# Kernel optimization log

Hardware: AMD Instinct MI355X
Metric: run time of the kernel (lower is better)

## Reference

```python
import jax, jax.numpy as jnp
import numpy as np

KH, KW = 2, 2          # kernel_size
STH, STW = 2, 2        # stride
NW = KH * KW           # num wires (qubits) per patch
DIM = 2 ** NW          # Hilbert-space dim = 16


def setup_inputs() -> dict:
    key = jax.random.key(0)
    k1, k2 = jax.random.split(key)
    x = jax.random.normal(k1, (32, 4, 64, 64), dtype=jnp.float32)
    # learned parameter: [in_channels, out_channels//numwires, 2^NW, 2^NW]
    params = jax.random.normal(k2, (4, 8, DIM, DIM), dtype=jnp.float32)
    return {"x": x, "params": params}


def _extract_patches(x):
    # x: [B, C, H, W] -> [B, C, px, py, KH*KW] (row-major kh,kw ordering,
    # matching patches.permute(0,1,4,5,2,3).flatten(4) in the original)
    B, C, H, W = x.shape
    px = (H - KH) // STH + 1
    py = (W - KW) // STW + 1
    rows = (jnp.arange(px) * STH)[:, None] + jnp.arange(KH)  # [px, KH]
    cols = (jnp.arange(py) * STW)[:, None] + jnp.arange(KW)  # [py, KW]
    p = x[:, :, rows][:, :, :, :, cols]        # [B, C, px, KH, py, KW]
    p = p.transpose(0, 1, 2, 4, 3, 5)          # [B, C, px, py, KH, KW]
    return p.reshape(B, C, px, py, NW), px, py


def _forward(x, params):
    B, C, H, W = x.shape
    p, px, py = _extract_patches(x)
    M = B * px * py
    theta = p.transpose(1, 0, 2, 3, 4).reshape(C, M, NW)  # 'b c px py i -> c (b px py) i'

    # Encode: the original builds the full tensor-product of per-wire RX
    # matrices and contracts with |0...0>, which selects row 0 of the Kronecker
    # product. Row 0 of RX(theta) is [cos(t/2), -i sin(t/2)], so the encoded
    # state is the Kronecker product of the per-wire row-0 vectors (same math,
    # without materializing the [C,M,16,16] unitary).
    half = theta * 0.5
    v = (jnp.cos(half).astype(jnp.complex64)[..., None] * jnp.array([1.0, 0.0], jnp.complex64)
         + jnp.sin(half).astype(jnp.complex64)[..., None] * jnp.array([0.0, -1.0j], jnp.complex64))  # [C,M,NW,2]
    state = v[:, :, 0]                                     # [C, M, 2]
    for w in range(1, NW):
        state = (state[..., :, None] * v[:, :, w][..., None, :]).reshape(C, M, -1)
    # state: [C, M, DIM]

    # Skew-Hermitian generator: real part antisymmetric, imag part symmetric.
    sym = params + params.swapaxes(-1, -2)
    asym = params - params.swapaxes(-1, -2)
    SH = asym.astype(jnp.complex64) + 1j * sym.astype(jnp.complex64)  # [C, D, DIM, DIM]
    U = jax.vmap(jax.vmap(jax.scipy.linalg.expm))(SH)                 # [C, D, DIM, DIM]

    y = jnp.einsum('cdij,cmi->cdmj', U, state)  # [C, D, M, DIM]

    # Decode: per-wire marginal probabilities -> <sigma_z>-style expectation -> acos
    probs = (y * jnp.conj(y)).real              # [C, D, M, DIM]
    D = probs.shape[1]
    outs = []
    for j in range(NW):
        marg = probs.reshape(C, D, M, 2 ** j, 2, 2 ** (NW - j - 1)).sum(axis=(3, 5))  # [C,D,M,2]
        outs.append(jnp.arccos(marg[..., 0] - marg[..., 1]))
    out = jnp.stack(outs, -1)                   # [C, D, M, NW]
    out = out.sum(0)                            # [D, M, NW]  (sum over in_channels)

    # 'c (b px py) (x y) -> b (c x y) px py' with c=D, x=KH, y=KW
    out = out.reshape(D, B, px, py, KH, KW).transpose(1, 0, 4, 5, 2, 3)
    return out.reshape(B, D * KH * KW, px, py)  # [B, out_channels, px, py]


def reference(x, params):
    return _forward(x, params)
```

## Files before the change

kernel.cpp:

```cpp
#include <hip/hip_runtime.h>
#include <math.h>


typedef __attribute__((ext_vector_type(8)))  short bf16x8;
typedef __attribute__((ext_vector_type(16))) float f32x16;

__device__ __forceinline__ unsigned bfr(float x) {
    unsigned u = __float_as_uint(x);
    return (u + 0x7FFFu + ((u >> 16) & 1u)) >> 16;
}

__device__ __forceinline__ void mm16(float2* D, const float2* A, const float2* B,
                                     int i, int j, int tid) {
    float accr = 0.f, acci = 0.f;
    #pragma unroll
    for (int t = 0; t < 16; ++t) {
        float2 a = A[i * 16 + t], b = B[t * 16 + j];
        accr += a.x * b.x - a.y * b.y;
        acci += a.x * b.y + a.y * b.x;
    }
    D[tid] = make_float2(accr, acci);
    __syncthreads();
}

__device__ __forceinline__ void mm16_addb(float2* D, const float2* A, const float2* B,
                                          const float2* X1, const float2* X2c,
                                          const float2* X3c,
                                          float b0, float b1, float b2, float b3,
                                          int i, int j, int tid) {
    float accr = 0.f, acci = 0.f;
    #pragma unroll
    for (int t = 0; t < 16; ++t) {
        float2 a = A[i * 16 + t], b = B[t * 16 + j];
        accr += a.x * b.x - a.y * b.y;
        acci += a.x * b.y + a.y * b.x;
    }
    float2 v1 = X1[tid], v2 = X2c[tid], v3 = X3c[tid];
    float idd = (i == j) ? 1.f : 0.f;
    accr += b0 * idd + b1 * v1.x + b2 * v2.x + b3 * v3.x;
    acci +=            b1 * v1.y + b2 * v2.y + b3 * v3.y;
    D[tid] = make_float2(accr, acci);
    __syncthreads();
}

__global__ __launch_bounds__(256) void prep_kernel(const float* __restrict__ params,
                                                   unsigned* __restrict__ wfrag) {
    __shared__ float2 Xs[256], X2[256], X3[256], X4[256], PA[256], PB[256];
    __shared__ float red[256];
    __shared__ float srow[16];
    __shared__ int ssexp;

    const int bid = blockIdx.x;
    const int tid = threadIdx.x;
    const int i = tid >> 4, j = tid & 15;

    const float* pm = params + bid * 256;
    float pij = pm[i * 16 + j];
    float pji = pm[j * 16 + i];
    float ar = pij - pji;
    float ai = pij + pji;
    red[tid] = fabsf(ar) + fabsf(ai);
    __syncthreads();
    if (j == 0) {
        float s = 0.f;
        for (int t = 0; t < 16; ++t) s += red[i * 16 + t];
        srow[i] = s;
    }
    __syncthreads();
    if (tid == 0) {
        float mx = 0.f;
        for (int t = 0; t < 16; ++t) mx = fmaxf(mx, srow[t]);
        int se = 0;
        while (mx > 1.0f && se < 40) { mx *= 0.5f; se++; }
        ssexp = se;
    }
    __syncthreads();
    const int sexp = ssexp;
    const float scale = exp2f((float)(-sexp));
    Xs[tid] = make_float2(ar * scale, ai * scale);
    __syncthreads();

    mm16(X2, Xs, Xs, i, j, tid);
    mm16(X3, X2, Xs, i, j, tid);
    mm16(X4, X2, X2, i, j, tid);

    {
        const float c8 = 2.4801587e-5f, c9 = 2.7557319e-6f, c10 = 2.7557319e-7f,
                    c11 = 2.5052108e-8f, c12 = 2.0876757e-9f;
        float2 v1 = Xs[tid], v2 = X2[tid], v3 = X3[tid], v4 = X4[tid];
        float idd = (i == j) ? 1.f : 0.f;
        PA[tid] = make_float2(c8 * idd + c9 * v1.x + c10 * v2.x + c11 * v3.x + c12 * v4.x,
                              c9 * v1.y + c10 * v2.y + c11 * v3.y + c12 * v4.y);
        __syncthreads();
    }
    mm16_addb(PB, X4, PA, Xs, X2, X3,
              4.1666667e-2f, 8.3333333e-3f, 1.3888889e-3f, 1.9841270e-4f, i, j, tid);
    mm16_addb(PA, X4, PB, Xs, X2, X3,
              1.f, 1.f, 0.5f, 1.6666667e-1f, i, j, tid);

    float2* cur = PA;
    float2* nxt = PB;
    for (int sq = 0; sq < sexp; ++sq) {
        float accr = 0.f, acci = 0.f;
        #pragma unroll
        for (int t = 0; t < 16; ++t) {
            float2 a = cur[i * 16 + t], b = cur[t * 16 + j];
            accr += a.x * b.x - a.y * b.y;
            acci += a.x * b.y + a.y * b.x;
        }
        nxt[tid] = make_float2(accr, acci);
        __syncthreads();
        float2* tmp = cur; cur = nxt; nxt = tmp;
    }

    float2 e = cur[tid];
    int pc = __popc(i) & 3;
    float2 o;
    if (pc == 0)      o = make_float2( e.x,  e.y);
    else if (pc == 1) o = make_float2( e.y, -e.x);
    else if (pc == 2) o = make_float2(-e.x, -e.y);
    else              o = make_float2(-e.y,  e.x);
    Xs[(tid & 15) * 16 + (tid >> 4)] = o;
    __syncthreads();

    {
        const int lane = tid & 63;
        const int pr = tid >> 6;
        const int row = lane & 31;
        const int kh = lane >> 5;
        const int k0 = kh * 8 + pr * 2;
        float v0, v1;
        if (row < 16) { v0 = Xs[row * 16 + k0].x; v1 = Xs[row * 16 + k0 + 1].x; }
        else          { v0 = Xs[(row - 16) * 16 + k0].y; v1 = Xs[(row - 16) * 16 + k0 + 1].y; }
        unsigned base = (unsigned)(bid * 64 + lane) * 4u;
        wfrag[base + pr] = bfr(v0) | (bfr(v1) << 16);
    }
}

__device__ __forceinline__ float acos_fast(float t) {
    float ax = fabsf(t);
    float p = fmaf(ax, -0.0187293f, 0.0742610f);
    p = fmaf(ax, p, -0.2121144f);
    p = fmaf(ax, p, 1.5707288f);
    float f = sqrtf(1.0f - ax) * p;
    return (t >= 0.f) ? f : (3.14159265358979f - f);
}

__global__ __launch_bounds__(256)
__attribute__((amdgpu_waves_per_eu(2, 4)))
void qconv_kernel(const float* __restrict__ x,
                  const unsigned* __restrict__ wfrag,
                  float* __restrict__ out) {
    const int tid = threadIdx.x;
    const int lane = tid & 63;
    const int s = lane & 31;
    const int hi = lane >> 5;
    const int wave = blockIdx.x * 4 + (tid >> 6);
    const int msite = wave >> 1;
    const int dh = wave & 1;
    const int m = msite * 32 + s;
    const int b = m >> 10, ix = (m >> 5) & 31, iy = m & 31;

    const bf16x8* wf = (const bf16x8*)wfrag;

    float2 xa[4], xb[4];
    #pragma unroll
    for (int c = 0; c < 4; ++c) {
        const float* xc = x + (((b * 4 + c) * 64 + 2 * ix) * 64 + 2 * iy);
        xa[c] = *(const float2*)xc;
        xb[c] = *(const float2*)(xc + 64);
    }
    bf16x8 wfr[16];
    #pragma unroll
    for (int dd = 0; dd < 4; ++dd)
        #pragma unroll
        for (int c = 0; c < 4; ++c)
            wfr[dd * 4 + c] = wf[(c * 8 + dh * 4 + dd) * 64 + lane];

    bf16x8 bhi[4], blo[4];
    #pragma unroll
    for (int c = 0; c < 4; ++c) {
        float sn0, cs0, sn1, cs1, sn2, cs2, sn3, cs3;
        __sincosf(xa[c].x * 0.5f, &sn0, &cs0);
        __sincosf(xa[c].y * 0.5f, &sn1, &cs1);
        __sincosf(xb[c].x * 0.5f, &sn2, &cs2);
        __sincosf(xb[c].y * 0.5f, &sn3, &cs3);
        float f0 = hi ? sn0 : cs0;
        float g0 = f0 * cs1, g1 = f0 * sn1;
        float h0 = g0 * cs2, h1 = g0 * sn2, h2 = g1 * cs2, h3 = g1 * sn2;
        float r[8];
        r[0] = h0 * cs3; r[1] = h0 * sn3; r[2] = h1 * cs3; r[3] = h1 * sn3;
        r[4] = h2 * cs3; r[5] = h2 * sn3; r[6] = h3 * cs3; r[7] = h3 * sn3;
        #pragma unroll
        for (int e = 0; e < 8; ++e) {
            unsigned hb = bfr(r[e]);
            bhi[c][e] = (short)hb;
            blo[c][e] = (short)bfr(r[e] - __uint_as_float(hb << 16));
        }
    }

    const float sgn1 = hi ? -1.f : 1.f;
    const f32x16 z = {0.f,0.f,0.f,0.f,0.f,0.f,0.f,0.f,
                      0.f,0.f,0.f,0.f,0.f,0.f,0.f,0.f};

    #pragma unroll
    for (int dd = 0; dd < 4; ++dd) {
        const int d = dh * 4 + dd;
        float accA = 0.f, accB = 0.f;
        #pragma unroll
        for (int c = 0; c < 4; ++c) {
            bf16x8 ahi = wfr[dd * 4 + c];
            f32x16 acc = __builtin_amdgcn_mfma_f32_32x32x16_bf16(ahi, blo[c], z, 0, 0, 0);
            acc = __builtin_amdgcn_mfma_f32_32x32x16_bf16(ahi, bhi[c], acc, 0, 0, 0);
            float q[8];
            #pragma unroll
            for (int i = 0; i < 8; ++i)
                q[i] = fmaf(acc[i], acc[i], acc[8 + i] * acc[8 + i]);
            float e01 = q[0] + q[1], o01 = q[0] - q[1];
            float e23 = q[2] + q[3], o23 = q[2] - q[3];
            float e45 = q[4] + q[5], o45 = q[4] - q[5];
            float e67 = q[6] + q[7], o67 = q[6] - q[7];
            float A  = e01 + e23, B2a = e01 - e23, A3a = o01 + o23;
            float C  = e45 + e67, B2b = e45 - e67, A3b = o45 + o67;
            float S   = A + C;
            float pw0 = A - C;
            float pw1 = sgn1 * S;
            float pw2 = B2a + B2b;
            float pw3 = A3a + A3b;
            float sendA = hi ? pw0 : pw2, myA = hi ? pw2 : pw0;
            float sendB = hi ? pw1 : pw3, myB = hi ? pw3 : pw1;
            float tA = myA + __shfl_xor(sendA, 32);
            float tB = myB + __shfl_xor(sendB, 32);
            tA = fminf(fmaxf(tA, -1.f), 1.f);
            tB = fminf(fmaxf(tB, -1.f), 1.f);
            accA += acos_fast(tA);
            accB += acos_fast(tB);
        }
        float* ob = out + ((b * 32 + d * 4 + 2 * hi) * 32 + ix) * 32 + iy;
        ob[0]    = accA;
        ob[1024] = accB;
    }
}

extern "C" void kernel_launch(void* const* d_in, const int* in_sizes, int n_in,
                              void* d_out, int out_size, void* d_ws, size_t ws_size,
                              hipStream_t stream) {
    const float* x = (const float*)d_in[0];
    const float* params = (const float*)d_in[1];
    float* out = (float*)d_out;
    unsigned* wfrag = (unsigned*)d_ws;

    prep_kernel<<<32, 256, 0, stream>>>(params, wfrag);
    qconv_kernel<<<512, 256, 0, stream>>>(x, wfrag, out);
}
```

Baseline: 21.52 us.

## Fuse prep and qconv into one cooperative kernel with a grid sync

Merges the matrix-exponential prep kernel and the main MFMA convolution kernel into one cooperative launch. Blocks 0-31 compute the unitary fragments, and every block loads and encodes its input patches before a grid-wide barrier, so encoding overlaps with prep. This removes one kernel launch and the gap between kernels. In exchange it adds a grid sync, a larger shared-memory footprint for every block, and an occupancy query on the host for each call. It falls back to two launches if cooperative launch is not possible.

```diff
diff --git a/kernel.cpp b/kernel.cpp
--- a/kernel.cpp
+++ b/kernel.cpp
@@ -1,5 +1,8 @@
 #include <hip/hip_runtime.h>
+#include <hip/hip_cooperative_groups.h>
 #include <math.h>
+
+namespace cg = cooperative_groups;
 
 
 typedef __attribute__((ext_vector_type(8)))  short bf16x8;
@@ -9,6 +12,13 @@
     unsigned u = __float_as_uint(x);
     return (u + 0x7FFFu + ((u >> 16) & 1u)) >> 16;
 }
+
+struct PrepSmem {
+    float2 Xs[256], X2[256], X3[256], X4[256], PA[256], PB[256];
+    float red[256];
+    float srow[16];
+    int ssexp;
+};
 
 __device__ __forceinline__ void mm16(float2* D, const float2* A, const float2* B,
                                      int i, int j, int tid) {
@@ -43,15 +53,19 @@
     __syncthreads();
 }
 
-__global__ __launch_bounds__(256) void prep_kernel(const float* __restrict__ params,
-                                                   unsigned* __restrict__ wfrag) {
-    __shared__ float2 Xs[256], X2[256], X3[256], X4[256], PA[256], PB[256];
-    __shared__ float red[256];
-    __shared__ float srow[16];
-    __shared__ int ssexp;
-
-    const int bid = blockIdx.x;
-    const int tid = threadIdx.x;
+__device__ __forceinline__ float acos_fast(float t) {
+    float ax = fabsf(t);
+    float p = fmaf(ax, -0.0187293f, 0.0742610f);
+    p = fmaf(ax, p, -0.2121144f);
+    p = fmaf(ax, p, 1.5707288f);
+    float f = sqrtf(1.0f - ax) * p;
+    return (t >= 0.f) ? f : (3.14159265358979f - f);
+}
+
+__device__ __forceinline__ void prep_body(PrepSmem& sm,
+                                          const float* __restrict__ params,
+                                          unsigned* __restrict__ wfrag,
+                                          int bid, int tid) {
     const int i = tid >> 4, j = tid & 15;
 
     const float* pm = params + bid * 256;
@@ -59,47 +73,47 @@
     float pji = pm[j * 16 + i];
     float ar = pij - pji;
     float ai = pij + pji;
-    red[tid] = fabsf(ar) + fabsf(ai);
+    sm.red[tid] = fabsf(ar) + fabsf(ai);
     __syncthreads();
     if (j == 0) {
         float s = 0.f;
-        for (int t = 0; t < 16; ++t) s += red[i * 16 + t];
-        srow[i] = s;
+        for (int t = 0; t < 16; ++t) s += sm.red[i * 16 + t];
+        sm.srow[i] = s;
     }
     __syncthreads();
     if (tid == 0) {
         float mx = 0.f;
-        for (int t = 0; t < 16; ++t) mx = fmaxf(mx, srow[t]);
+        for (int t = 0; t < 16; ++t) mx = fmaxf(mx, sm.srow[t]);
         int se = 0;
         while (mx > 1.0f && se < 40) { mx *= 0.5f; se++; }
-        ssexp = se;
-    }
-    __syncthreads();
-    const int sexp = ssexp;
+        sm.ssexp = se;
+    }
+    __syncthreads();
+    const int sexp = sm.ssexp;
     const float scale = exp2f((float)(-sexp));
-    Xs[tid] = make_float2(ar * scale, ai * scale);
-    __syncthreads();
-
-    mm16(X2, Xs, Xs, i, j, tid);
-    mm16(X3, X2, Xs, i, j, tid);
-    mm16(X4, X2, X2, i, j, tid);
+    sm.Xs[tid] = make_float2(ar * scale, ai * scale);
+    __syncthreads();
+
+    mm16(sm.X2, sm.Xs, sm.Xs, i, j, tid);
+    mm16(sm.X3, sm.X2, sm.Xs, i, j, tid);
+    mm16(sm.X4, sm.X2, sm.X2, i, j, tid);
 
     {
         const float c8 = 2.4801587e-5f, c9 = 2.7557319e-6f, c10 = 2.7557319e-7f,
                     c11 = 2.5052108e-8f, c12 = 2.0876757e-9f;
-        float2 v1 = Xs[tid], v2 = X2[tid], v3 = X3[tid], v4 = X4[tid];
+        float2 v1 = sm.Xs[tid], v2 = sm.X2[tid], v3 = sm.X3[tid], v4 = sm.X4[tid];
         float idd = (i == j) ? 1.f : 0.f;
-        PA[tid] = make_float2(c8 * idd + c9 * v1.x + c10 * v2.x + c11 * v3.x + c12 * v4.x,
-                              c9 * v1.y + c10 * v2.y + c11 * v3.y + c12 * v4.y);
+        sm.PA[tid] = make_float2(c8 * idd + c9 * v1.x + c10 * v2.x + c11 * v3.x + c12 * v4.x,
+                                 c9 * v1.y + c10 * v2.y + c11 * v3.y + c12 * v4.y);
         __syncthreads();
     }
-    mm16_addb(PB, X4, PA, Xs, X2, X3,
+    mm16_addb(sm.PB, sm.X4, sm.PA, sm.Xs, sm.X2, sm.X3,
               4.1666667e-2f, 8.3333333e-3f, 1.3888889e-3f, 1.9841270e-4f, i, j, tid);
-    mm16_addb(PA, X4, PB, Xs, X2, X3,
+    mm16_addb(sm.PA, sm.X4, sm.PB, sm.Xs, sm.X2, sm.X3,
               1.f, 1.f, 0.5f, 1.6666667e-1f, i, j, tid);
 
-    float2* cur = PA;
-    float2* nxt = PB;
+    float2* cur = sm.PA;
+    float2* nxt = sm.PB;
     for (int sq = 0; sq < sexp; ++sq) {
         float accr = 0.f, acci = 0.f;
         #pragma unroll
@@ -120,7 +134,7 @@
     else if (pc == 1) o = make_float2( e.y, -e.x);
     else if (pc == 2) o = make_float2(-e.x, -e.y);
     else              o = make_float2(-e.y,  e.x);
-    Xs[(tid & 15) * 16 + (tid >> 4)] = o;
+    sm.Xs[(tid & 15) * 16 + (tid >> 4)] = o;
     __syncthreads();
 
     {
@@ -130,61 +144,37 @@
         const int kh = lane >> 5;
         const int k0 = kh * 8 + pr * 2;
         float v0, v1;
-        if (row < 16) { v0 = Xs[row * 16 + k0].x; v1 = Xs[row * 16 + k0 + 1].x; }
-        else          { v0 = Xs[(row - 16) * 16 + k0].y; v1 = Xs[(row - 16) * 16 + k0 + 1].y; }
+        if (row < 16) { v0 = sm.Xs[row * 16 + k0].x; v1 = sm.Xs[row * 16 + k0 + 1].x; }
+        else          { v0 = sm.Xs[(row - 16) * 16 + k0].y; v1 = sm.Xs[(row - 16) * 16 + k0 + 1].y; }
         unsigned base = (unsigned)(bid * 64 + lane) * 4u;
         wfrag[base + pr] = bfr(v0) | (bfr(v1) << 16);
     }
 }
 
-__device__ __forceinline__ float acos_fast(float t) {
-    float ax = fabsf(t);
-    float p = fmaf(ax, -0.0187293f, 0.0742610f);
-    p = fmaf(ax, p, -0.2121144f);
-    p = fmaf(ax, p, 1.5707288f);
-    float f = sqrtf(1.0f - ax) * p;
-    return (t >= 0.f) ? f : (3.14159265358979f - f);
-}
-
-__global__ __launch_bounds__(256)
-__attribute__((amdgpu_waves_per_eu(2, 4)))
-void qconv_kernel(const float* __restrict__ x,
-                  const unsigned* __restrict__ wfrag,
-                  float* __restrict__ out) {
-    const int tid = threadIdx.x;
-    const int lane = tid & 63;
+__device__ __forceinline__ void qconv_build(const float* __restrict__ x,
+                                            int blkid, int tid,
+                                            bf16x8 (&bhi)[4], bf16x8 (&blo)[4],
+                                            int& lane, int& hi, int& dh,
+                                            int& b, int& ix, int& iy) {
+    lane = tid & 63;
     const int s = lane & 31;
-    const int hi = lane >> 5;
-    const int wave = blockIdx.x * 4 + (tid >> 6);
+    hi = lane >> 5;
+    const int wave = blkid * 4 + (tid >> 6);
     const int msite = wave >> 1;
-    const int dh = wave & 1;
+    dh = wave & 1;
     const int m = msite * 32 + s;
-    const int b = m >> 10, ix = (m >> 5) & 31, iy = m & 31;
-
-    const bf16x8* wf = (const bf16x8*)wfrag;
-
-    float2 xa[4], xb[4];
+    b = m >> 10; ix = (m >> 5) & 31; iy = m & 31;
+
     #pragma unroll
     for (int c = 0; c < 4; ++c) {
         const float* xc = x + (((b * 4 + c) * 64 + 2 * ix) * 64 + 2 * iy);
-        xa[c] = *(const float2*)xc;
-        xb[c] = *(const float2*)(xc + 64);
-    }
-    bf16x8 wfr[16];
-    #pragma unroll
-    for (int dd = 0; dd < 4; ++dd)
-        #pragma unroll
-        for (int c = 0; c < 4; ++c)
-            wfr[dd * 4 + c] = wf[(c * 8 + dh * 4 + dd) * 64 + lane];
-
-    bf16x8 bhi[4], blo[4];
-    #pragma unroll
-    for (int c = 0; c < 4; ++c) {
+        float2 xa = *(const float2*)xc;
+        float2 xb = *(const float2*)(xc + 64);
         float sn0, cs0, sn1, cs1, sn2, cs2, sn3, cs3;
-        __sincosf(xa[c].x * 0.5f, &sn0, &cs0);
-        __sincosf(xa[c].y * 0.5f, &sn1, &cs1);
-        __sincosf(xb[c].x * 0.5f, &sn2, &cs2);
-        __sincosf(xb[c].y * 0.5f, &sn3, &cs3);
+        __sincosf(xa.x * 0.5f, &sn0, &cs0);
+        __sincosf(xa.y * 0.5f, &sn1, &cs1);
+        __sincosf(xb.x * 0.5f, &sn2, &cs2);
+        __sincosf(xb.y * 0.5f, &sn3, &cs3);
         float f0 = hi ? sn0 : cs0;
         float g0 = f0 * cs1, g1 = f0 * sn1;
         float h0 = g0 * cs2, h1 = g0 * sn2, h2 = g1 * cs2, h3 = g1 * sn2;
@@ -198,6 +188,20 @@
             blo[c][e] = (short)bfr(r[e] - __uint_as_float(hb << 16));
         }
     }
+}
+
+__device__ __forceinline__ void qconv_mfma(const unsigned* __restrict__ wfrag,
+                                           float* __restrict__ out,
+                                           const bf16x8 (&bhi)[4], const bf16x8 (&blo)[4],
+                                           int lane, int hi, int dh,
+                                           int b, int ix, int iy) {
+    const bf16x8* wf = (const bf16x8*)wfrag;
+    bf16x8 wfr[16];
+    #pragma unroll
+    for (int dd = 0; dd < 4; ++dd)
+        #pragma unroll
+        for (int c = 0; c < 4; ++c)
+            wfr[dd * 4 + c] = wf[(c * 8 + dh * 4 + dd) * 64 + lane];
 
     const float sgn1 = hi ? -1.f : 1.f;
     const f32x16 z = {0.f,0.f,0.f,0.f,0.f,0.f,0.f,0.f,
@@ -242,6 +246,46 @@
     }
 }
 
+__global__ __launch_bounds__(256)
+__attribute__((amdgpu_waves_per_eu(2, 4)))
+void fused_kernel(const float* __restrict__ x,
+                  const float* __restrict__ params,
+                  unsigned* __restrict__ wfrag,
+                  float* __restrict__ out) {
+    __shared__ PrepSmem sm;
+    const int tid = threadIdx.x;
+
+    if (blockIdx.x < 32) {
+        prep_body(sm, params, wfrag, blockIdx.x, tid);
+        __threadfence();
+    }
+
+    int lane, hi, dh, b, ix, iy;
+    bf16x8 bhi[4], blo[4];
+    qconv_build(x, blockIdx.x, tid, bhi, blo, lane, hi, dh, b, ix, iy);
+
+    cg::this_grid().sync();
+
+    qconv_mfma(wfrag, out, bhi, blo, lane, hi, dh, b, ix, iy);
+}
+
+__global__ __launch_bounds__(256) void prep_kernel(const float* __restrict__ params,
+                                                   unsigned* __restrict__ wfrag) {
+    __shared__ PrepSmem sm;
+    prep_body(sm, params, wfrag, blockIdx.x, threadIdx.x);
+}
+
+__global__ __launch_bounds__(256)
+__attribute__((amdgpu_waves_per_eu(2, 4)))
+void qconv_kernel(const float* __restrict__ x,
+                  const unsigned* __restrict__ wfrag,
+                  float* __restrict__ out) {
+    int lane, hi, dh, b, ix, iy;
+    bf16x8 bhi[4], blo[4];
+    qconv_build(x, blockIdx.x, threadIdx.x, bhi, blo, lane, hi, dh, b, ix, iy);
+    qconv_mfma(wfrag, out, bhi, blo, lane, hi, dh, b, ix, iy);
+}
+
 extern "C" void kernel_launch(void* const* d_in, const int* in_sizes, int n_in,
                               void* d_out, int out_size, void* d_ws, size_t ws_size,
                               hipStream_t stream) {
@@ -250,6 +294,19 @@
     float* out = (float*)d_out;
     unsigned* wfrag = (unsigned*)d_ws;
 
-    prep_kernel<<<32, 256, 0, stream>>>(params, wfrag);
-    qconv_kernel<<<512, 256, 0, stream>>>(x, wfrag, out);
-}
+    int blocksPerCU = 0;
+    hipError_t qerr = hipOccupancyMaxActiveBlocksPerMultiprocessor(
+        &blocksPerCU, (const void*)fused_kernel, 256, 0);
+    bool coop = (qerr == hipSuccess) && (blocksPerCU * 256 >= 512);
+
+    if (coop) {
+        void* args[] = {(void*)&x, (void*)&params, (void*)&wfrag, (void*)&out};
+        hipError_t lerr = hipLaunchCooperativeKernel((void*)fused_kernel, dim3(512),
+                                                     dim3(256), args, 0, stream);
+        coop = (lerr == hipSuccess);
+    }
+    if (!coop) {
+        prep_kernel<<<32, 256, 0, stream>>>(params, wfrag);
+        qconv_kernel<<<512, 256, 0, stream>>>(x, wfrag, out);
+    }
+}
```

Result: no change. 21.85 us (+1.5%).
